# Optimization experiments

Hardware: AMD Instinct MI355X
Metric: run time of the kernel (lower is better)

The kernel has to match this reference:

```python
import jax, jax.numpy as jnp
import numpy as np

D_MODEL = 2048
NUM_HEADS = 16
KV_HEADS = 4
HEAD_DIM = D_MODEL // NUM_HEADS  # 128
SEQ = 4096
BATCH = 1
ROPE_THETA = 10000.0


def _rope_cache(T, dim, base, dtype):
    inv_freq = 1.0 / (base ** (jnp.arange(0, dim, 2, dtype=jnp.float32) / dim))
    t = jnp.arange(T, dtype=jnp.float32)
    freqs = jnp.outer(t, inv_freq)                      # (T, dim/2)
    emb = jnp.concatenate([freqs, freqs], axis=-1)      # (T, dim)
    return jnp.cos(emb).astype(dtype), jnp.sin(emb).astype(dtype)


def _rotate_half(x):
    d = x.shape[-1] // 2
    return jnp.concatenate([-x[..., d:], x[..., :d]], axis=-1)


def _apply_rope(q, k, cos, sin):
    # q: (B,T,Hq,D), k: (B,T,Hkv,D); cos/sin: (T,D) broadcast over heads
    c = cos[None, :, None, :]
    s = sin[None, :, None, :]
    q = q * c + _rotate_half(q) * s
    k = k * c + _rotate_half(k) * s
    return q, k


def setup_inputs() -> dict:
    key = jax.random.key(0)
    ks = jax.random.split(key, 6)
    sc = 1.0 / np.sqrt(D_MODEL)
    kv_out = KV_HEADS * HEAD_DIM
    return {
        "x": jax.random.normal(ks[0], (BATCH, SEQ, D_MODEL), dtype=jnp.float32),
        "Wq": jax.random.normal(ks[1], (D_MODEL, D_MODEL), dtype=jnp.float32) * sc,
        "Wk": jax.random.normal(ks[2], (D_MODEL, kv_out), dtype=jnp.float32) * sc,
        "Wv": jax.random.normal(ks[3], (D_MODEL, kv_out), dtype=jnp.float32) * sc,
        "Wo": jax.random.normal(ks[4], (D_MODEL, D_MODEL), dtype=jnp.float32) * sc,
        "bo": jax.random.normal(ks[5], (D_MODEL,), dtype=jnp.float32) * 0.01,
    }


def reference(x, Wq, Wk, Wv, Wo, bo):
    B, T, _ = x.shape
    q = (x @ Wq).reshape(B, T, NUM_HEADS, HEAD_DIM)
    k = (x @ Wk).reshape(B, T, KV_HEADS, HEAD_DIM)
    v = (x @ Wv).reshape(B, T, KV_HEADS, HEAD_DIM)

    cos, sin = _rope_cache(T, HEAD_DIM, ROPE_THETA, x.dtype)
    q, k = _apply_rope(q, k, cos, sin)

    reps = NUM_HEADS // KV_HEADS
    k = jnp.repeat(k, reps, axis=2)  # repeat_interleave on head dim
    v = jnp.repeat(v, reps, axis=2)

    # (B,H,T,D)
    q = q.transpose(0, 2, 1, 3)
    k = k.transpose(0, 2, 1, 3)
    v = v.transpose(0, 2, 1, 3)

    scores = jnp.einsum("bhqd,bhkd->bhqk", q, k)
    causal = jnp.triu(jnp.ones((T, T), dtype=bool), k=1)
    scores = jnp.where(causal[None, None], -jnp.inf, scores)
    attn = jax.nn.softmax(scores / jnp.sqrt(jnp.asarray(HEAD_DIM, x.dtype)), axis=-1)

    ctx = jnp.einsum("bhqk,bhkd->bhqd", attn, v)
    ctx = ctx.transpose(0, 2, 1, 3).reshape(B, T, D_MODEL)
    return ctx @ Wo + bo
```

## Files before the change

### kernel.cpp

```cpp
#include <hip/hip_runtime.h>
#include <cstdint>
#include <cstddef>

#define SEQ 4096
#define DM  2048
#define NH  16
#define KVH 4
#define HD  128

typedef short bf16_t;
typedef __attribute__((ext_vector_type(8))) short bf16x8;
typedef __attribute__((ext_vector_type(4))) float f32x4;

__device__ __forceinline__ bf16_t f2b(float f) {
  unsigned u = __builtin_bit_cast(unsigned, f);
  u += 0x7fffu + ((u >> 16) & 1u);
  return (bf16_t)(u >> 16);
}
__device__ __forceinline__ float b2f(bf16_t s) {
  unsigned u = ((unsigned)(unsigned short)s) << 16;
  return __builtin_bit_cast(float, u);
}

__device__ __forceinline__ void gload_lds16(const void* gsrc, void* ldst) {
  __builtin_amdgcn_global_load_lds(
      (__attribute__((address_space(1))) void*)gsrc,
      (__attribute__((address_space(3))) void*)ldst, 16, 0, 0);
}

__global__ void cast_x_bf16(const float* __restrict__ x, bf16_t* __restrict__ xb, int n4) {
  int i = blockIdx.x * 256 + threadIdx.x;
  if (i >= n4) return;
  float4 v = ((const float4*)x)[i];
  union { bf16_t h[4]; unsigned long long u; } o;
  o.h[0] = f2b(v.x); o.h[1] = f2b(v.y); o.h[2] = f2b(v.z); o.h[3] = f2b(v.w);
  ((unsigned long long*)xb)[i] = o.u;
}

__global__ void transpose_cast_w(const float* __restrict__ W, bf16_t* __restrict__ Wt,
                                 int K, int N) {
  __shared__ float tile[32][33];
  int k0 = blockIdx.y * 32, n0 = blockIdx.x * 32;
  int tx = threadIdx.x, ty = threadIdx.y;
#pragma unroll
  for (int dy = 0; dy < 32; dy += 8)
    tile[ty + dy][tx] = W[(size_t)(k0 + ty + dy) * N + n0 + tx];
  __syncthreads();
#pragma unroll
  for (int dy = 0; dy < 32; dy += 8)
    Wt[(size_t)(n0 + ty + dy) * K + k0 + tx] = f2b(tile[tx][ty + dy]);
}

__global__ void rope_tab(float* __restrict__ ct, float* __restrict__ st) {
  int i = blockIdx.x * 256 + threadIdx.x;
  if (i >= SEQ * 64) return;
  int t = i >> 6, j = i & 63;
  float invf = expf(-(float)j * (9.210340371976184f / 64.0f));
  float ang = (float)t * invf;
  ct[i] = cosf(ang);
  st[i] = sinf(ang);
}

__global__ void rope_apply(bf16_t* __restrict__ Qb, bf16_t* __restrict__ KVb,
                           const float* __restrict__ ct, const float* __restrict__ st) {
  int i = blockIdx.x * 256 + threadIdx.x;
  const int qtot = SEQ * NH * 64;
  const int tot = qtot + SEQ * KVH * 64;
  if (i >= tot) return;
  bf16_t* base; int t, j;
  if (i < qtot) {
    t = i >> 10; int rem = i & 1023; int hh = rem >> 6; j = rem & 63;
    base = Qb + (size_t)t * DM + hh * HD;
  } else {
    int i2 = i - qtot;
    t = i2 >> 8; int rem = i2 & 255; int hh = rem >> 6; j = rem & 63;
    base = KVb + (size_t)t * 1024 + hh * HD;
  }
  float c = ct[t * 64 + j], s = st[t * 64 + j];
  float x0 = b2f(base[j]);
  float x1 = b2f(base[j + 64]);
  base[j]      = f2b(x0 * c - x1 * s);
  base[j + 64] = f2b(x1 * c + x0 * s);
}

__global__ void transpose_v(const bf16_t* __restrict__ KVb, bf16_t* __restrict__ Vt) {
  __shared__ bf16_t tile[32][33];
  int t0 = blockIdx.y * 32, d0 = blockIdx.x * 32;
  int tx = threadIdx.x, ty = threadIdx.y;
#pragma unroll
  for (int dy = 0; dy < 32; dy += 8)
    tile[ty + dy][tx] = KVb[(size_t)(t0 + ty + dy) * 1024 + 512 + d0 + tx];
  __syncthreads();
#pragma unroll
  for (int dy = 0; dy < 32; dy += 8)
    Vt[(size_t)(d0 + ty + dy) * SEQ + t0 + tx] = tile[tx][ty + dy];
}

template <int BIAS>
__global__ __launch_bounds__(256, 2)
void gemm_bt(const bf16_t* __restrict__ A, const bf16_t* __restrict__ Bt,
             void* __restrict__ Cout, const float* __restrict__ bias,
             int M, int N, int K) {
  __shared__ __align__(16) bf16_t ldsA[128 * 64];
  __shared__ __align__(16) bf16_t ldsB[128 * 64];
  const int t = threadIdx.x;
  const int w = t >> 6, l = t & 63;
  const int lg = l >> 4, lr = l & 15;
  const int bm = blockIdx.y, bn = blockIdx.x;
  const int wr = (w >> 1) * 64, wc = (w & 1) * 64;

  f32x4 acc[4][4] = {};

  for (int k0 = 0; k0 < K; k0 += 64) {
    __syncthreads();
#pragma unroll
    for (int i = 0; i < 4; ++i) {
      int idx = i * 256 + t;
      int row = idx >> 3;
      int ch  = (idx & 7) ^ (row & 7);
      gload_lds16(A  + (size_t)(bm * 128 + row) * K + k0 + ch * 8, &ldsA[idx * 8]);
      gload_lds16(Bt + (size_t)(bn * 128 + row) * K + k0 + ch * 8, &ldsB[idx * 8]);
    }
    __syncthreads();
#pragma unroll
    for (int kk = 0; kk < 2; ++kk) {
      bf16x8 af[4], bfr[4];
#pragma unroll
      for (int m = 0; m < 4; ++m) {
        int row = wr + m * 16 + lr;
        int ch = (kk * 4 + lg) ^ (row & 7);
        af[m] = *(const bf16x8*)&ldsA[row * 64 + ch * 8];
      }
#pragma unroll
      for (int n = 0; n < 4; ++n) {
        int row = wc + n * 16 + lr;
        int ch = (kk * 4 + lg) ^ (row & 7);
        bfr[n] = *(const bf16x8*)&ldsB[row * 64 + ch * 8];
      }
#pragma unroll
      for (int m = 0; m < 4; ++m)
#pragma unroll
        for (int n = 0; n < 4; ++n)
          acc[m][n] = __builtin_amdgcn_mfma_f32_16x16x32_bf16(af[m], bfr[n], acc[m][n], 0, 0, 0);
    }
  }

  const int row0 = bm * 128 + wr + lg * 4;
  const int col0 = bn * 128 + wc + lr;
  if (BIAS) {
    float* C = (float*)Cout;
#pragma unroll
    for (int n = 0; n < 4; ++n) {
      int col = col0 + n * 16;
      float b = bias[col];
#pragma unroll
      for (int m = 0; m < 4; ++m)
#pragma unroll
        for (int r = 0; r < 4; ++r)
          C[(size_t)(row0 + m * 16 + r) * N + col] = acc[m][n][r] + b;
    }
  } else {
    bf16_t* C = (bf16_t*)Cout;
#pragma unroll
    for (int m = 0; m < 4; ++m)
#pragma unroll
      for (int n = 0; n < 4; ++n) {
        int col = col0 + n * 16;
#pragma unroll
        for (int r = 0; r < 4; ++r)
          C[(size_t)(row0 + m * 16 + r) * N + col] = f2b(acc[m][n][r]);
      }
  }
}

__global__ __launch_bounds__(256, 2)
void attn_fwd(const bf16_t* __restrict__ Qb, const bf16_t* __restrict__ KVb,
              const bf16_t* __restrict__ Vt, bf16_t* __restrict__ ctx) {
  __shared__ __align__(16) bf16_t kt[2][64 * 128];
  __shared__ __align__(16) bf16_t vts[2][128 * 64];
  __shared__ __align__(16) bf16_t plds[4][2][16 * 64];

  const int t = threadIdx.x;
  const int w = t >> 6, l = t & 63;
  const int lg = l >> 4, lr = l & 15;
  const int h = blockIdx.y, g = h >> 2;
  const int b = blockIdx.x;
  const int qt0 = b, qt1 = 63 - b;

  bf16x8 qf[2][4];
#pragma unroll
  for (int kk = 0; kk < 4; ++kk) {
    qf[0][kk] = *(const bf16x8*)&Qb[(size_t)(qt0 * 64 + w * 16 + lr) * DM + h * HD + kk * 32 + lg * 8];
    qf[1][kk] = *(const bf16x8*)&Qb[(size_t)(qt1 * 64 + w * 16 + lr) * DM + h * HD + kk * 32 + lg * 8];
  }

  f32x4 acc[2][9] = {};
  float m_run[2][4];
#pragma unroll
  for (int m = 0; m < 2; ++m)
#pragma unroll
    for (int r = 0; r < 4; ++r) m_run[m][r] = -1e30f;

  bf16x8 ones;
#pragma unroll
  for (int i = 0; i < 8; ++i) ones[i] = (short)0x3F80;

  const float sl2e = 0.08838834764831845f * 1.4426950408889634f;

  const bf16_t* ksrc = KVb + g * 128;
  const bf16_t* vsrc = Vt + (size_t)(g * 128) * SEQ;
  auto stage = [&](int buf, int kvt) {
#pragma unroll
    for (int i = 0; i < 4; ++i) {
      int idx = i * 256 + t;
      int row = idx >> 4;
      int ch = (idx & 15) ^ (row & 7);
      gload_lds16(ksrc + (size_t)(kvt * 64 + row) * 1024 + ch * 8, &kt[buf][idx * 8]);
    }
#pragma unroll
    for (int i = 0; i < 4; ++i) {
      int idx = i * 256 + t;
      int row = idx >> 3;
      int ch = (idx & 7) ^ (row & 7);
      gload_lds16(vsrc + (size_t)row * SEQ + kvt * 64 + ch * 8, &vts[buf][idx * 8]);
    }
  };

  const int nkv = qt1 + 1;
  stage(0, 0);

  for (int kv = 0; kv < nkv; ++kv) {
    const int cur = kv & 1;
    const int kv0 = kv * 64;
    __syncthreads();
    if (kv + 1 < nkv) stage(cur ^ 1, kv + 1);

    const bool act0 = kv <= qt0;

    f32x4 s[2][4];
#pragma unroll
    for (int m = 0; m < 2; ++m)
#pragma unroll
      for (int n = 0; n < 4; ++n) s[m][n] = f32x4{0.f, 0.f, 0.f, 0.f};

    __builtin_amdgcn_s_setprio(1);
#pragma unroll
    for (int n = 0; n < 4; ++n) {
      int row = n * 16 + lr;
#pragma unroll
      for (int kk = 0; kk < 4; ++kk) {
        int ch = (kk * 4 + lg) ^ (row & 7);
        bf16x8 kf = *(const bf16x8*)&kt[cur][row * 128 + ch * 8];
        if (act0) s[0][n] = __builtin_amdgcn_mfma_f32_16x16x32_bf16(qf[0][kk], kf, s[0][n], 0, 0, 0);
        s[1][n] = __builtin_amdgcn_mfma_f32_16x16x32_bf16(qf[1][kk], kf, s[1][n], 0, 0, 0);
      }
    }
    __builtin_amdgcn_s_setprio(0);

#pragma unroll
    for (int m = 0; m < 2; ++m) {
      if (m == 0 && !act0) continue;
      const int qtm = (m == 0) ? qt0 : qt1;

      if (kv == qtm) {
#pragma unroll
        for (int n = 0; n < 4; ++n)
#pragma unroll
          for (int r = 0; r < 4; ++r) {
            int key = kv0 + n * 16 + lr;
            int qrow = qtm * 64 + w * 16 + lg * 4 + r;
            if (key > qrow) s[m][n][r] = -1e30f;
          }
      }

      float pmax[4];
#pragma unroll
      for (int r = 0; r < 4; ++r)
        pmax[r] = fmaxf(fmaxf(s[m][0][r], s[m][1][r]), fmaxf(s[m][2][r], s[m][3][r]));
#pragma unroll
      for (int off = 1; off < 16; off <<= 1)
#pragma unroll
        for (int r = 0; r < 4; ++r)
          pmax[r] = fmaxf(pmax[r], __shfl_xor(pmax[r], off, 64));

      bool need = false;
#pragma unroll
      for (int r = 0; r < 4; ++r) need |= (pmax[r] > m_run[m][r] + 60.f);
      if (__any((int)need)) {
        float alpha[4];
#pragma unroll
        for (int r = 0; r < 4; ++r) {
          float mn = fmaxf(m_run[m][r], pmax[r]);
          alpha[r] = exp2f((m_run[m][r] - mn) * sl2e);
          m_run[m][r] = mn;
        }
#pragma unroll
        for (int nd = 0; nd < 9; ++nd)
#pragma unroll
          for (int r = 0; r < 4; ++r)
            acc[m][nd][r] *= alpha[r];
      }

#pragma unroll
      for (int n = 0; n < 4; ++n)
#pragma unroll
        for (int r = 0; r < 4; ++r) {
          float p = exp2f((s[m][n][r] - m_run[m][r]) * sl2e);
          int row = lg * 4 + r;
          int col = n * 16 + lr;
          int ch = (col >> 3) ^ (row & 7);
          plds[w][m][row * 64 + ch * 8 + (col & 7)] = f2b(p);
        }
    }

#pragma unroll
    for (int kk2 = 0; kk2 < 2; ++kk2) {
      int pch = (kk2 * 4 + lg) ^ (lr & 7);
      bf16x8 pf0 = *(const bf16x8*)&plds[w][0][lr * 64 + pch * 8];
      bf16x8 pf1 = *(const bf16x8*)&plds[w][1][lr * 64 + pch * 8];
      __builtin_amdgcn_s_setprio(1);
#pragma unroll
      for (int nd = 0; nd < 8; ++nd) {
        int vrow = nd * 16 + lr;
        int vch = (kk2 * 4 + lg) ^ (vrow & 7);
        bf16x8 vf = *(const bf16x8*)&vts[cur][vrow * 64 + vch * 8];
        if (act0) acc[0][nd] = __builtin_amdgcn_mfma_f32_16x16x32_bf16(pf0, vf, acc[0][nd], 0, 0, 0);
        acc[1][nd] = __builtin_amdgcn_mfma_f32_16x16x32_bf16(pf1, vf, acc[1][nd], 0, 0, 0);
      }
      if (act0) acc[0][8] = __builtin_amdgcn_mfma_f32_16x16x32_bf16(pf0, ones, acc[0][8], 0, 0, 0);
      acc[1][8] = __builtin_amdgcn_mfma_f32_16x16x32_bf16(pf1, ones, acc[1][8], 0, 0, 0);
      __builtin_amdgcn_s_setprio(0);
    }
  }

#pragma unroll
  for (int m = 0; m < 2; ++m) {
    const int qtm = (m == 0) ? qt0 : qt1;
#pragma unroll
    for (int r = 0; r < 4; ++r) {
      float rl = 1.0f / acc[m][8][r];
      int qrow = qtm * 64 + w * 16 + lg * 4 + r;
#pragma unroll
      for (int nd = 0; nd < 8; ++nd) {
        int col = h * HD + nd * 16 + lr;
        ctx[(size_t)qrow * DM + col] = f2b(acc[m][nd][r] * rl);
      }
    }
  }
}

extern "C" void kernel_launch(void* const* d_in, const int* in_sizes, int n_in,
                              void* d_out, int out_size, void* d_ws, size_t ws_size,
                              hipStream_t stream) {
  const float* x  = (const float*)d_in[0];
  const float* Wq = (const float*)d_in[1];
  const float* Wk = (const float*)d_in[2];
  const float* Wv = (const float*)d_in[3];
  const float* Wo = (const float*)d_in[4];
  const float* bo = (const float*)d_in[5];
  float* out = (float*)d_out;

  char* p = (char*)d_ws;
  bf16_t* xb   = (bf16_t*)p;
  bf16_t* ctx  = xb;
  p += (size_t)SEQ * DM * 2;
  bf16_t* Wqt  = (bf16_t*)p; p += (size_t)DM * DM * 2;
  bf16_t* Wkvt = (bf16_t*)p; p += (size_t)1024 * DM * 2;
  bf16_t* Wot  = (bf16_t*)p; p += (size_t)DM * DM * 2;
  bf16_t* Qb   = (bf16_t*)p; p += (size_t)SEQ * DM * 2;
  bf16_t* KVb  = (bf16_t*)p; p += (size_t)SEQ * 1024 * 2;
  bf16_t* Vt   = (bf16_t*)p; p += (size_t)512 * SEQ * 2;
  float*  ctab = (float*)p;  p += (size_t)SEQ * 64 * 4;
  float*  stab = (float*)p;  p += (size_t)SEQ * 64 * 4;

  cast_x_bf16<<<(SEQ * DM / 4 + 255) / 256, 256, 0, stream>>>(x, xb, SEQ * DM / 4);
  transpose_cast_w<<<dim3(DM / 32, DM / 32), dim3(32, 8), 0, stream>>>(Wq, Wqt, DM, DM);
  transpose_cast_w<<<dim3(512 / 32, DM / 32), dim3(32, 8), 0, stream>>>(Wk, Wkvt, DM, 512);
  transpose_cast_w<<<dim3(512 / 32, DM / 32), dim3(32, 8), 0, stream>>>(Wv, Wkvt + (size_t)512 * DM, DM, 512);
  transpose_cast_w<<<dim3(DM / 32, DM / 32), dim3(32, 8), 0, stream>>>(Wo, Wot, DM, DM);
  rope_tab<<<(SEQ * 64 + 255) / 256, 256, 0, stream>>>(ctab, stab);

  gemm_bt<0><<<dim3(DM / 128, SEQ / 128), 256, 0, stream>>>(xb, Wqt, Qb, nullptr, SEQ, DM, DM);
  gemm_bt<0><<<dim3(1024 / 128, SEQ / 128), 256, 0, stream>>>(xb, Wkvt, KVb, nullptr, SEQ, 1024, DM);

  rope_apply<<<(SEQ * (NH + KVH) * 64 + 255) / 256, 256, 0, stream>>>(Qb, KVb, ctab, stab);
  transpose_v<<<dim3(512 / 32, SEQ / 32), dim3(32, 8), 0, stream>>>(KVb, Vt);

  attn_fwd<<<dim3(32, NH), 256, 0, stream>>>(Qb, KVb, Vt, ctx);

  gemm_bt<1><<<dim3(DM / 128, SEQ / 128), 256, 0, stream>>>(ctx, Wot, out, bo, SEQ, DM, DM);
}
```

Measured before the change: 312.4 us.

## Transpose QK^T MFMA so each lane holds one query row, pack P stores

Swaps the MFMA operand order so the score tile comes out transposed, with each lane owning a single query row and four consecutive keys. This cuts the row-max reduction to two cross-lane shuffles and lets each lane keep one running max instead of four. The P tile is written to LDS as packed 64-bit stores under a new swizzle rather than scalar 16-bit stores. The rescale path now needs extra shuffles to redistribute alpha back to the accumulator layout.

```diff
diff --git a/kernel.cpp b/kernel.cpp
--- a/kernel.cpp
+++ b/kernel.cpp
@@ -195,17 +195,14 @@
   }
 
   f32x4 acc[2][9] = {};
-  float m_run[2][4];
-#pragma unroll
-  for (int m = 0; m < 2; ++m)
-#pragma unroll
-    for (int r = 0; r < 4; ++r) m_run[m][r] = -1e30f;
+  float m_run[2] = {-1e30f, -1e30f};
 
   bf16x8 ones;
 #pragma unroll
   for (int i = 0; i < 8; ++i) ones[i] = (short)0x3F80;
 
   const float sl2e = 0.08838834764831845f * 1.4426950408889634f;
+  const int swz = (lr & 7) << 1;
 
   const bf16_t* ksrc = KVb + g * 128;
   const bf16_t* vsrc = Vt + (size_t)(g * 128) * SEQ;
@@ -251,8 +248,8 @@
       for (int kk = 0; kk < 4; ++kk) {
         int ch = (kk * 4 + lg) ^ (row & 7);
         bf16x8 kf = *(const bf16x8*)&kt[cur][row * 128 + ch * 8];
-        if (act0) s[0][n] = __builtin_amdgcn_mfma_f32_16x16x32_bf16(qf[0][kk], kf, s[0][n], 0, 0, 0);
-        s[1][n] = __builtin_amdgcn_mfma_f32_16x16x32_bf16(qf[1][kk], kf, s[1][n], 0, 0, 0);
+        if (act0) s[0][n] = __builtin_amdgcn_mfma_f32_16x16x32_bf16(kf, qf[0][kk], s[0][n], 0, 0, 0);
+        s[1][n] = __builtin_amdgcn_mfma_f32_16x16x32_bf16(kf, qf[1][kk], s[1][n], 0, 0, 0);
       }
     }
     __builtin_amdgcn_s_setprio(0);
@@ -261,39 +258,34 @@
     for (int m = 0; m < 2; ++m) {
       if (m == 0 && !act0) continue;
       const int qtm = (m == 0) ? qt0 : qt1;
+      const int qrow = qtm * 64 + w * 16 + lr;
 
       if (kv == qtm) {
 #pragma unroll
         for (int n = 0; n < 4; ++n)
 #pragma unroll
           for (int r = 0; r < 4; ++r) {
-            int key = kv0 + n * 16 + lr;
-            int qrow = qtm * 64 + w * 16 + lg * 4 + r;
+            int key = kv0 + n * 16 + lg * 4 + r;
             if (key > qrow) s[m][n][r] = -1e30f;
           }
       }
 
-      float pmax[4];
-#pragma unroll
-      for (int r = 0; r < 4; ++r)
-        pmax[r] = fmaxf(fmaxf(s[m][0][r], s[m][1][r]), fmaxf(s[m][2][r], s[m][3][r]));
-#pragma unroll
-      for (int off = 1; off < 16; off <<= 1)
+      float pm0 = fmaxf(fmaxf(s[m][0][0], s[m][0][1]), fmaxf(s[m][0][2], s[m][0][3]));
+      float pm1 = fmaxf(fmaxf(s[m][1][0], s[m][1][1]), fmaxf(s[m][1][2], s[m][1][3]));
+      float pm2 = fmaxf(fmaxf(s[m][2][0], s[m][2][1]), fmaxf(s[m][2][2], s[m][2][3]));
+      float pm3 = fmaxf(fmaxf(s[m][3][0], s[m][3][1]), fmaxf(s[m][3][2], s[m][3][3]));
+      float pm = fmaxf(fmaxf(pm0, pm1), fmaxf(pm2, pm3));
+      pm = fmaxf(pm, __shfl_xor(pm, 16, 64));
+      pm = fmaxf(pm, __shfl_xor(pm, 32, 64));
+
+      if (__any((int)(pm > m_run[m] + 60.f))) {
+        float mn = fmaxf(m_run[m], pm);
+        float a_s = exp2f((m_run[m] - mn) * sl2e);
+        m_run[m] = mn;
+        float alpha[4];
 #pragma unroll
         for (int r = 0; r < 4; ++r)
-          pmax[r] = fmaxf(pmax[r], __shfl_xor(pmax[r], off, 64));
-
-      bool need = false;
-#pragma unroll
-      for (int r = 0; r < 4; ++r) need |= (pmax[r] > m_run[m][r] + 60.f);
-      if (__any((int)need)) {
-        float alpha[4];
-#pragma unroll
-        for (int r = 0; r < 4; ++r) {
-          float mn = fmaxf(m_run[m][r], pmax[r]);
-          alpha[r] = exp2f((m_run[m][r] - mn) * sl2e);
-          m_run[m][r] = mn;
-        }
+          alpha[r] = __shfl(a_s, (l & 48) | (lg * 4 + r), 64);
 #pragma unroll
         for (int nd = 0; nd < 9; ++nd)
 #pragma unroll
@@ -302,22 +294,21 @@
       }
 
 #pragma unroll
-      for (int n = 0; n < 4; ++n)
-#pragma unroll
-        for (int r = 0; r < 4; ++r) {
-          float p = exp2f((s[m][n][r] - m_run[m][r]) * sl2e);
-          int row = lg * 4 + r;
-          int col = n * 16 + lr;
-          int ch = (col >> 3) ^ (row & 7);
-          plds[w][m][row * 64 + ch * 8 + (col & 7)] = f2b(p);
-        }
+      for (int n = 0; n < 4; ++n) {
+        union { bf16_t h[4]; unsigned long long u; } pk;
+#pragma unroll
+        for (int r = 0; r < 4; ++r)
+          pk.h[r] = f2b(exp2f((s[m][n][r] - m_run[m]) * sl2e));
+        int gr = (n * 4 + lg) ^ swz;
+        *(unsigned long long*)&plds[w][m][lr * 64 + gr * 4] = pk.u;
+      }
     }
 
 #pragma unroll
     for (int kk2 = 0; kk2 < 2; ++kk2) {
-      int pch = (kk2 * 4 + lg) ^ (lr & 7);
-      bf16x8 pf0 = *(const bf16x8*)&plds[w][0][lr * 64 + pch * 8];
-      bf16x8 pf1 = *(const bf16x8*)&plds[w][1][lr * 64 + pch * 8];
+      int gg = ((kk2 * 8 + lg * 2) ^ swz);
+      bf16x8 pf0 = *(const bf16x8*)&plds[w][0][lr * 64 + gg * 4];
+      bf16x8 pf1 = *(const bf16x8*)&plds[w][1][lr * 64 + gg * 4];
       __builtin_amdgcn_s_setprio(1);
 #pragma unroll
       for (int nd = 0; nd < 8; ++nd) {
```

Result: faster. 299.9 us (-4.0%).
